# Performance work log

Hardware: AMD Instinct MI355X
Metric: run time of the kernel (lower is better)

Reference implementation:

```python
import jax, jax.numpy as jnp
import numpy as np

B = 8192; NPG = 32; N = B * NPG; E = 4 * N
F_IN = 70; HEADS = 2; HOUT = 64; D = HEADS * HOUT; NB = 4; REL = 86; DK = D // 2
NEG_SLOPE = 0.2; EPS = 1e-5


def setup_inputs():
    key = jax.random.key(0)
    ks = list(jax.random.split(key, 32)); ki = iter(ks)
    def nk():
        return next(ki)
    def rn(shape, s=0.1):
        return jax.random.normal(nk(), shape, jnp.float32) * s
    base = (jnp.arange(E) // (E // B)) * NPG  # each graph owns a contiguous node range
    def edges():
        s = base + jax.random.randint(nk(), (E,), 0, NPG)
        d = base + jax.random.randint(nk(), (E,), 0, NPG)
        return jnp.stack([s, d]).astype(jnp.int32)
    return dict(
        xh=rn((N, F_IN), 1.0), xt=rn((N, F_IN), 1.0),
        edge_h=edges(), edge_t=edges(),
        batch=(jnp.arange(N) // NPG).astype(jnp.int32),
        rels=jax.random.randint(nk(), (B,), 0, REL).astype(jnp.int32),
        W0=rn((F_IN, D)), Wr=rn((NB - 1, D, D)),
        att_src=rn((NB, HEADS, HOUT)), att_dst=rn((NB, HEADS, HOUT)),
        gat_b=jnp.zeros((NB, D), jnp.float32),
        sag_rel_w=rn((NB, D)), sag_rel_b=jnp.zeros((NB,), jnp.float32),
        sag_root_w=rn((NB, D)),
        nw=jnp.ones((NB, D), jnp.float32), nb2=jnp.zeros((NB, D), jnp.float32),
        inw=jnp.ones((F_IN,), jnp.float32), inb=jnp.zeros((F_IN,), jnp.float32),
        wq=rn((D, DK)), wk=rn((D, DK)),
        cob=jnp.zeros((DK,), jnp.float32), coa=rn((DK,)),
        rel_emb=rn((REL, D * D)),
    )


def _lnorm(x, w, b):  # PyG LayerNorm, node mode (per-node over features)
    mu = jnp.mean(x, -1, keepdims=True)
    var = jnp.var(x, -1, keepdims=True)
    return (x - mu) * jax.lax.rsqrt(var + EPS) * w + b


def _gat(x, src, dst, W, a_s, a_d, bias):
    # src/dst already include self-loops (PyG GATConv default add_self_loops=True)
    h = (x @ W).reshape(N, HEADS, HOUT)
    a_src = jnp.einsum('nhc,hc->nh', h, a_s)
    a_dst = jnp.einsum('nhc,hc->nh', h, a_d)
    alpha = jax.nn.leaky_relu(a_src[src] + a_dst[dst], NEG_SLOPE)  # [E+N, H]
    m = jax.ops.segment_max(alpha, dst, num_segments=N)
    ex = jnp.exp(alpha - m[dst])
    den = jax.ops.segment_sum(ex, dst, num_segments=N)
    w = ex / (den[dst] + 1e-16)
    out = jax.ops.segment_sum(h[src] * w[:, :, None], dst, num_segments=N)
    return out.reshape(N, D) + bias


def _readout(x, ei, batch, rw, rb, root_w):
    # SAGPooling(min_score=-1): GraphConv score, per-graph softmax, keeps all nodes
    aggr = jax.ops.segment_sum(x[ei[0]], ei[1], num_segments=N)
    score = aggr @ rw + rb + x @ root_w  # [N]
    m = jax.ops.segment_max(score, batch, num_segments=B)
    ex = jnp.exp(score - m[batch])
    den = jax.ops.segment_sum(ex, batch, num_segments=B)
    s = ex / (den[batch] + 1e-16)
    return jax.ops.segment_sum(x * s[:, None], batch, num_segments=B)  # global_add_pool [B, D]


def _l2norm(x):
    return x / jnp.clip(jnp.linalg.norm(x, axis=-1, keepdims=True), 1e-12)


def _forward(xh, xt, edge_h, edge_t, batch, rels, W0, Wr, att_src, att_dst, gat_b,
             sag_rel_w, sag_rel_b, sag_root_w, nw, nb2, inw, inb, wq, wk, cob, coa, rel_emb):
    loops = jnp.arange(N, dtype=edge_h.dtype)
    def side(x, ei):
        src = jnp.concatenate([ei[0], loops])
        dst = jnp.concatenate([ei[1], loops])
        x = _lnorm(x, inw, inb)
        reprs = []
        for i in range(NB):
            W = W0 if i == 0 else Wr[i - 1]
            x = _gat(x, src, dst, W, att_src[i], att_dst[i], gat_b[i])
            reprs.append(_readout(x, ei, batch, sag_rel_w[i], sag_rel_b[i], sag_root_w[i]))
            x = jax.nn.elu(_lnorm(x, nw[i], nb2[i]))
        return jnp.stack(reprs, axis=-2)  # [B, NB, D]

    rh = side(xh, edge_h)
    rt = side(xt, edge_t)

    # CoAttentionLayer(receiver=heads, attendant=tails)
    keys = rh @ wk       # [B, NB, DK]
    queries = rt @ wq    # [B, NB, DK]
    att = jnp.tanh(keys[:, :, None, :] + queries[:, None, :, :] + cob) @ coa  # [B, NB, NB]

    # RESCAL
    r = _l2norm(rel_emb[rels]).reshape(B, D, D)
    h = _l2norm(rh)
    t = _l2norm(rt)
    scores = jnp.einsum('bid,bde,bje->bij', h, r, t)
    return jnp.sum(att * scores, axis=(-2, -1))  # [B]


def reference(xh, xt, edge_h, edge_t, batch, rels, W0, Wr, att_src, att_dst, gat_b,
              sag_rel_w, sag_rel_b, sag_root_w, nw, nb2, inw, inb, wq, wk, cob, coa, rel_emb):
    return _forward(xh, xt, edge_h, edge_t, batch, rels, W0, Wr, att_src, att_dst, gat_b,
                    sag_rel_w, sag_rel_b, sag_root_w, nw, nb2, inw, inb, wq, wk, cob, coa, rel_emb)
```

## Files before the change

### kernel.cpp

```cpp
#include <hip/hip_runtime.h>
#include <math.h>

#define NG 8192
#define NPG 32
#define NN (NG*NPG)
#define NE (NN*4)
#define EPG 128
#define NEL (EPG+NPG)
#define FIN 70
#define DIM 128
#define XS 132
#define TS 36
#define NB 4
#define DK 64
#define NREL 86

typedef __attribute__((ext_vector_type(8))) short short8;
typedef __attribute__((ext_vector_type(4))) float f32x4;
typedef __attribute__((ext_vector_type(4))) unsigned int u32x4;

__device__ inline unsigned cvtpk(float a, float b) {
  unsigned r;
  asm("v_cvt_pk_bf16_f32 %0, %1, %2" : "=v"(r) : "v"(a), "v"(b));
  return r;
}
__device__ inline float lo16f(unsigned u) { return __uint_as_float(u << 16); }
__device__ inline float hi16f(unsigned u) { return __uint_as_float(u & 0xffff0000u); }
__device__ inline float bf16f(unsigned short h) {
  return __uint_as_float(((unsigned int)h) << 16);
}

__device__ inline void split8(const f32x4& a, const f32x4& b, short8& hi, short8& lo) {
  u32x4 H, L;
  #pragma unroll
  for (int p = 0; p < 2; ++p) {
    float x0 = a[2*p], x1 = a[2*p+1];
    unsigned h = cvtpk(x0, x1);
    H[p] = h;
    L[p] = cvtpk(x0 - lo16f(h), x1 - hi16f(h));
  }
  #pragma unroll
  for (int p = 0; p < 2; ++p) {
    float x0 = b[2*p], x1 = b[2*p+1];
    unsigned h = cvtpk(x0, x1);
    H[2+p] = h;
    L[2+p] = cvtpk(x0 - lo16f(h), x1 - hi16f(h));
  }
  hi = __builtin_bit_cast(short8, H);
  lo = __builtin_bit_cast(short8, L);
}

__device__ inline short8 ld8(const unsigned short* p) {
  union { short8 s; uint2 u[2]; } U;
  U.u[0] = *(const uint2*)p;
  U.u[1] = *(const uint2*)(p + 4);
  return U.s;
}

struct Smem {
  float x[NPG][XS];
  unsigned short h2thi[DIM][TS];
  unsigned short h2tlo[DIM][TS];
  union {
    struct {
      float Pt[2][NPG][TS];
      float alpha[2][NEL];
    } a;
    struct {
      float keysl[NB][DK];
      float querl[NB][DK];
      float attw[NB*NB];
      float red[NB*NB];
      float u4[4][DIM];
    } f;
  } uu;
  int   srcl[EPG];
  int   dstl[EPG];
  float asrc[NPG][2];
  float adst[NPG][2];
  float den[NPG][2];
  float mh[2];
  float wred[4][2];
  float pl[NPG];
  float ql[NPG];
  float sval[NPG];
  float sacc[NPG];
  float repr[2][NB][DIM];
  float scl[2][NB];
};

__global__ __launch_bounds__(256) void relnorm_kernel(
    const float* __restrict__ re, float* __restrict__ outn) {
  int r = blockIdx.x;
  const float* row = re + (size_t)r * (DIM*DIM);
  float s = 0.f;
  for (int i = threadIdx.x; i < DIM*DIM; i += 256) { float v = row[i]; s += v*v; }
  for (int w = 1; w < 64; w <<= 1) s += __shfl_xor(s, w);
  __shared__ float sred[4];
  if ((threadIdx.x & 63) == 0) sred[threadIdx.x >> 6] = s;
  __syncthreads();
  if (threadIdx.x == 0) outn[r] = sqrtf(sred[0]+sred[1]+sred[2]+sred[3]);
}

__global__ __launch_bounds__(256, 3) void ssi_kernel(
    const float* __restrict__ xh, const float* __restrict__ xt,
    const int* __restrict__ eh, const int* __restrict__ et,
    const int* __restrict__ rels,
    const float* __restrict__ W0, const float* __restrict__ Wr,
    const float* __restrict__ att_src, const float* __restrict__ att_dst,
    const float* __restrict__ gat_b,
    const float* __restrict__ srw, const float* __restrict__ srb,
    const float* __restrict__ sroot,
    const float* __restrict__ nw, const float* __restrict__ nb2,
    const float* __restrict__ inw, const float* __restrict__ inb,
    const float* __restrict__ wqm, const float* __restrict__ wkm,
    const float* __restrict__ cob, const float* __restrict__ coa,
    const float* __restrict__ rel_emb, const float* __restrict__ rnorm,
    float* __restrict__ out)
{
  __shared__ Smem sm;
  const int t = threadIdx.x;
  const int g = blockIdx.x;
  const int n0 = g * NPG;
  const int lw = t & 63;
  const int r0 = lw & 15;
  const int g4 = lw >> 4;
  const int nb = (t >> 6) * 32;
  const int hdw = t >> 7;

  for (int side = 0; side < 2; ++side) {
    const float* xin = side ? xt : xh;
    const int*   ed  = side ? et : eh;

    if (t < EPG) {
      sm.srcl[t] = ed[g*EPG + t] - n0;
      sm.dstl[t] = ed[NE + g*EPG + t] - n0;
    }
    {
      int n = t >> 3, j = t & 7;
      float s = 0.f, s2 = 0.f;
      for (int f = j; f < FIN; f += 8) {
        float v = xin[(size_t)(n0+n)*FIN + f];
        s += v; s2 += v*v;
      }
      for (int w = 1; w < 8; w <<= 1) { s += __shfl_xor(s, w); s2 += __shfl_xor(s2, w); }
      float mu  = s * (1.f/FIN);
      float var = s2 * (1.f/FIN) - mu*mu;
      float inv = rsqrtf(var + 1e-5f);
      for (int f = j; f < FIN; f += 8) {
        float v = xin[(size_t)(n0+n)*FIN + f];
        sm.x[n][f] = (v - mu) * inv * inw[f] + inb[f];
      }
      for (int f = FIN + j; f < 96; f += 8) sm.x[n][f] = 0.f;
    }
    __syncthreads();

    for (int li = 0; li < NB; ++li) {
      {
        const float* W = (li == 0) ? W0 : (Wr + (size_t)(li-1)*DIM*DIM);
        const int K  = (li == 0) ? FIN : DIM;
        const int KS = (li == 0) ? 3 : 4;
        f32x4 acc[2][2];
        #pragma unroll
        for (int mt = 0; mt < 2; ++mt)
          #pragma unroll
          for (int nt = 0; nt < 2; ++nt)
            acc[mt][nt] = (f32x4){0.f,0.f,0.f,0.f};
        for (int ks = 0; ks < KS; ++ks) {
          const int k0 = ks*32 + g4*8;
          short8 ah[2], al[2], bh[2], bl[2];
          #pragma unroll
          for (int mt = 0; mt < 2; ++mt) {
            f32x4 va = *(const f32x4*)&sm.x[mt*16 + r0][k0];
            f32x4 vb = *(const f32x4*)&sm.x[mt*16 + r0][k0+4];
            split8(va, vb, ah[mt], al[mt]);
          }
          #pragma unroll
          for (int nt = 0; nt < 2; ++nt) {
            const int c = nb + nt*16 + r0;
            f32x4 wa, wb;
            #pragma unroll
            for (int j = 0; j < 4; ++j) {
              int ka = k0 + j, kb = k0 + 4 + j;
              wa[j] = (ka < K) ? W[(size_t)ka*DIM + c] : 0.f;
              wb[j] = (kb < K) ? W[(size_t)kb*DIM + c] : 0.f;
            }
            split8(wa, wb, bh[nt], bl[nt]);
          }
          #pragma unroll
          for (int mt = 0; mt < 2; ++mt)
            #pragma unroll
            for (int nt = 0; nt < 2; ++nt) {
              acc[mt][nt] = __builtin_amdgcn_mfma_f32_16x16x32_bf16(ah[mt], bh[nt], acc[mt][nt], 0,0,0);
              acc[mt][nt] = __builtin_amdgcn_mfma_f32_16x16x32_bf16(ah[mt], bl[nt], acc[mt][nt], 0,0,0);
              acc[mt][nt] = __builtin_amdgcn_mfma_f32_16x16x32_bf16(al[mt], bh[nt], acc[mt][nt], 0,0,0);
              acc[mt][nt] = __builtin_amdgcn_mfma_f32_16x16x32_bf16(al[mt], bl[nt], acc[mt][nt], 0,0,0);
            }
        }
        #pragma unroll
        for (int mt = 0; mt < 2; ++mt)
          #pragma unroll
          for (int nt = 0; nt < 2; ++nt) {
            const int c = nb + nt*16 + r0;
            const int row0 = mt*16 + g4*4;
            f32x4 a = acc[mt][nt];
            unsigned h0 = cvtpk(a[0], a[1]), h1 = cvtpk(a[2], a[3]);
            unsigned l0 = cvtpk(a[0]-lo16f(h0), a[1]-hi16f(h0));
            unsigned l1 = cvtpk(a[2]-lo16f(h1), a[3]-hi16f(h1));
            *(uint2*)&sm.h2thi[c][row0] = make_uint2(h0, h1);
            *(uint2*)&sm.h2tlo[c][row0] = make_uint2(l0, l1);
          }
      }
      __syncthreads();

      {
        int n = t >> 3, hd = (t >> 2) & 1, j = t & 3;
        const float* as = att_src + ((size_t)li*2 + hd)*64;
        const float* ad = att_dst + ((size_t)li*2 + hd)*64;
        float ss = 0.f, sd = 0.f;
        #pragma unroll
        for (int u2 = 0; u2 < 16; ++u2) {
          int cl = u2*4 + j;
          int c = hd*64 + cl;
          float hv = bf16f(sm.h2thi[c][n]) + bf16f(sm.h2tlo[c][n]);
          ss += hv * as[cl];
          sd += hv * ad[cl];
        }
        ss += __shfl_xor(ss,1); ss += __shfl_xor(ss,2);
        sd += __shfl_xor(sd,1); sd += __shfl_xor(sd,2);
        if (j == 0) { sm.asrc[n][hd] = ss; sm.adst[n][hd] = sd; }
        float* Pz = &sm.uu.a.Pt[0][0][0];
        for (int idx = t; idx < 2*NPG*TS; idx += 256) Pz[idx] = 0.f;
      }
      __syncthreads();

      if (t < NEL) {
        int s = (t < EPG) ? sm.srcl[t] : (t - EPG);
        int d = (t < EPG) ? sm.dstl[t] : (t - EPG);
        #pragma unroll
        for (int hd = 0; hd < 2; ++hd) {
          float a = sm.asrc[s][hd] + sm.adst[d][hd];
          sm.uu.a.alpha[hd][t] = (a > 0.f) ? a : 0.2f*a;
        }
      }
      __syncthreads();

      {
        float a0 = (t < NEL) ? sm.uu.a.alpha[0][t] : -1e30f;
        float a1 = (t < NEL) ? sm.uu.a.alpha[1][t] : -1e30f;
        for (int w = 1; w < 64; w <<= 1) {
          a0 = fmaxf(a0, __shfl_xor(a0, w));
          a1 = fmaxf(a1, __shfl_xor(a1, w));
        }
        if ((t & 63) == 0) { sm.wred[t>>6][0] = a0; sm.wred[t>>6][1] = a1; }
      }
      __syncthreads();
      if (t < 2) {
        sm.mh[t] = fmaxf(fmaxf(sm.wred[0][t], sm.wred[1][t]),
                         fmaxf(sm.wred[2][t], sm.wred[3][t]));
      }
      __syncthreads();

      if (t < NEL) {
        int s = (t < EPG) ? sm.srcl[t] : (t - EPG);
        int d = (t < EPG) ? sm.dstl[t] : (t - EPG);
        float e0 = expf(sm.uu.a.alpha[0][t] - sm.mh[0]);
        float e1 = expf(sm.uu.a.alpha[1][t] - sm.mh[1]);
        atomicAdd(&sm.uu.a.Pt[0][d][s], e0);
        atomicAdd(&sm.uu.a.Pt[1][d][s], e1);
      }
      __syncthreads();

      if (t < 64) {
        int d = t & 31, hd = t >> 5;
        float s = 0.f;
        #pragma unroll
        for (int s4 = 0; s4 < NPG; s4 += 4) {
          f32x4 v = *(const f32x4*)&sm.uu.a.Pt[hd][d][s4];
          s += v[0] + v[1] + v[2] + v[3];
        }
        sm.den[d][hd] = 1.f / (s + 1e-16f);
      }
      __syncthreads();

      {
        int hd = t >> 7, r = (t >> 2) & 31, s0 = (t & 3) * 8;
        f32x4 pa = *(const f32x4*)&sm.uu.a.Pt[hd][r][s0];
        f32x4 pb = *(const f32x4*)&sm.uu.a.Pt[hd][r][s0+4];
        float dv = sm.den[r][hd];
        #pragma unroll
        for (int q = 0; q < 4; ++q) { pa[q] *= dv; pb[q] *= dv; }
        __syncthreads();
        unsigned short* Pu = (unsigned short*)&sm.uu.a.Pt[0][0][0];
        const int LO = 2*NPG*TS;
        int base = (hd*NPG + r)*TS + s0;
        unsigned h0 = cvtpk(pa[0], pa[1]), h1 = cvtpk(pa[2], pa[3]);
        unsigned h2_ = cvtpk(pb[0], pb[1]), h3 = cvtpk(pb[2], pb[3]);
        unsigned l0 = cvtpk(pa[0]-lo16f(h0), pa[1]-hi16f(h0));
        unsigned l1 = cvtpk(pa[2]-lo16f(h1), pa[3]-hi16f(h1));
        unsigned l2 = cvtpk(pb[0]-lo16f(h2_), pb[1]-hi16f(h2_));
        unsigned l3 = cvtpk(pb[2]-lo16f(h3), pb[3]-hi16f(h3));
        *(uint2*)(Pu + base)     = make_uint2(h0, h1);
        *(uint2*)(Pu + base + 4) = make_uint2(h2_, h3);
        *(uint2*)(Pu + LO + base)     = make_uint2(l0, l1);
        *(uint2*)(Pu + LO + base + 4) = make_uint2(l2, l3);
      }
      __syncthreads();

      {
        const unsigned short* Pu = (const unsigned short*)&sm.uu.a.Pt[0][0][0];
        const int LO = 2*NPG*TS;
        const int k0 = g4*8;
        f32x4 acc[2][2];
        #pragma unroll
        for (int mt = 0; mt < 2; ++mt)
          #pragma unroll
          for (int nt = 0; nt < 2; ++nt)
            acc[mt][nt] = (f32x4){0.f,0.f,0.f,0.f};
        short8 Ah[2], Al[2], Bh[2], Bl[2];
        #pragma unroll
        for (int mt = 0; mt < 2; ++mt) {
          int base = (hdw*NPG + mt*16 + r0)*TS + k0;
          Ah[mt] = ld8(Pu + base);
          Al[mt] = ld8(Pu + LO + base);
        }
        #pragma unroll
        for (int nt = 0; nt < 2; ++nt) {
          const int c = nb + nt*16 + r0;
          Bh[nt] = ld8(&sm.h2thi[c][k0]);
          Bl[nt] = ld8(&sm.h2tlo[c][k0]);
        }
        #pragma unroll
        for (int mt = 0; mt < 2; ++mt)
          #pragma unroll
          for (int nt = 0; nt < 2; ++nt) {
            acc[mt][nt] = __builtin_amdgcn_mfma_f32_16x16x32_bf16(Ah[mt], Bh[nt], acc[mt][nt], 0,0,0);
            acc[mt][nt] = __builtin_amdgcn_mfma_f32_16x16x32_bf16(Ah[mt], Bl[nt], acc[mt][nt], 0,0,0);
            acc[mt][nt] = __builtin_amdgcn_mfma_f32_16x16x32_bf16(Al[mt], Bh[nt], acc[mt][nt], 0,0,0);
          }
        #pragma unroll
        for (int nt = 0; nt < 2; ++nt) {
          const int c = nb + nt*16 + r0;
          float bc = gat_b[(size_t)li*DIM + c];
          #pragma unroll
          for (int mt = 0; mt < 2; ++mt)
            #pragma unroll
            for (int q = 0; q < 4; ++q)
              sm.x[mt*16 + g4*4 + q][c] = acc[mt][nt][q] + bc;
        }
      }
      __syncthreads();

      {
        int n = t >> 3, j = t & 7;
        const float* rw = srw   + (size_t)li*DIM;
        const float* ro = sroot + (size_t)li*DIM;
        float p = 0.f, q = 0.f;
        #pragma unroll
        for (int u2 = 0; u2 < 16; ++u2) {
          int c = u2*8 + j;
          float xv = sm.x[n][c];
          p += xv * rw[c];
          q += xv * ro[c];
        }
        for (int w = 1; w < 8; w <<= 1) { p += __shfl_xor(p,w); q += __shfl_xor(q,w); }
        if (j == 0) { sm.pl[n] = p; sm.ql[n] = q; }
        if (t < NPG) sm.sacc[t] = 0.f;
      }
      __syncthreads();

      if (t < EPG) atomicAdd(&sm.sacc[sm.dstl[t]], sm.pl[sm.srcl[t]]);
      __syncthreads();

      if (t < NPG) {
        float s = sm.sacc[t] + srb[li] + sm.ql[t];
        float m = s;
        for (int w = 1; w < 32; w <<= 1) m = fmaxf(m, __shfl_xor(m, w));
        float ex = expf(s - m);
        float dn = ex;
        for (int w = 1; w < 32; w <<= 1) dn += __shfl_xor(dn, w);
        sm.sval[t] = ex / (dn + 1e-16f);
      }
      __syncthreads();

      if (t < DIM) {
        float a = 0.f;
        for (int n = 0; n < NPG; ++n) a += sm.x[n][t] * sm.sval[n];
        sm.repr[side][li][t] = a;
      }
      __syncthreads();

      if (li < NB-1) {
        int n = t >> 3, j = t & 7;
        float s = 0.f, s2 = 0.f;
        #pragma unroll
        for (int u2 = 0; u2 < 16; ++u2) {
          float v = sm.x[n][u2*8 + j];
          s += v; s2 += v*v;
        }
        for (int w = 1; w < 8; w <<= 1) { s += __shfl_xor(s,w); s2 += __shfl_xor(s2,w); }
        float mu  = s * (1.f/DIM);
        float var = s2 * (1.f/DIM) - mu*mu;
        float inv = rsqrtf(var + 1e-5f);
        const float* wv = nw  + (size_t)li*DIM;
        const float* bv = nb2 + (size_t)li*DIM;
        #pragma unroll
        for (int u2 = 0; u2 < 16; ++u2) {
          int c = u2*8 + j;
          float v = (sm.x[n][c] - mu) * inv * wv[c] + bv[c];
          sm.x[n][c] = (v > 0.f) ? v : expm1f(v);
        }
        __syncthreads();
      }
    }
  }

  {
    int i2 = t >> 6, k = t & 63;
    float ak = 0.f, aq = 0.f;
    for (int d = 0; d < DIM; ++d) {
      ak += sm.repr[0][i2][d] * wkm[(size_t)d*DK + k];
      aq += sm.repr[1][i2][d] * wqm[(size_t)d*DK + k];
    }
    sm.uu.f.keysl[i2][k] = ak;
    sm.uu.f.querl[i2][k] = aq;
  }
  {
    int sd = t >> 7, i = (t >> 5) & 3, j2 = t & 31;
    float s = 0.f;
    #pragma unroll
    for (int u2 = 0; u2 < 4; ++u2) {
      float v = sm.repr[sd][i][j2*4+u2];
      s += v*v;
    }
    for (int w = 1; w < 32; w <<= 1) s += __shfl_xor(s, w);
    if (j2 == 0) sm.scl[sd][i] = 1.f / fmaxf(sqrtf(s), 1e-12f);
  }
  __syncthreads();

  {
    int pair = t >> 4, kk = t & 15;
    int i = pair >> 2, j = pair & 3;
    float a = 0.f;
    #pragma unroll
    for (int u2 = 0; u2 < 4; ++u2) {
      int k = kk*4+u2;
      a += tanhf(sm.uu.f.keysl[i][k] + sm.uu.f.querl[j][k] + cob[k]) * coa[k];
    }
    for (int w = 1; w < 16; w <<= 1) a += __shfl_xor(a, w);
    if (kk == 0) sm.uu.f.attw[pair] = a;
  }
  int rel = rels[g];
  if (t < DIM) {
    const float* rr = rel_emb + (size_t)rel * (DIM*DIM);
    float a0=0.f, a1=0.f, a2=0.f, a3=0.f;
    for (int d = 0; d < DIM; ++d) {
      float rv = rr[(size_t)d*DIM + t];
      a0 += sm.repr[0][0][d] * rv;
      a1 += sm.repr[0][1][d] * rv;
      a2 += sm.repr[0][2][d] * rv;
      a3 += sm.repr[0][3][d] * rv;
    }
    sm.uu.f.u4[0][t]=a0; sm.uu.f.u4[1][t]=a1; sm.uu.f.u4[2][t]=a2; sm.uu.f.u4[3][t]=a3;
  }
  __syncthreads();

  {
    float rninv = 1.f / fmaxf(rnorm[rel], 1e-12f);
    int pair = t >> 4, kk = t & 15;
    int i = pair >> 2, j = pair & 3;
    float a = 0.f;
    #pragma unroll
    for (int u2 = 0; u2 < 8; ++u2) {
      int e = kk*8+u2;
      a += sm.uu.f.u4[i][e] * sm.repr[1][j][e];
    }
    for (int w = 1; w < 16; w <<= 1) a += __shfl_xor(a, w);
    if (kk == 0)
      sm.uu.f.red[pair] = sm.uu.f.attw[pair] * a * sm.scl[0][i] * sm.scl[1][j] * rninv;
  }
  __syncthreads();
  if (t == 0) {
    float s = 0.f;
    for (int p = 0; p < NB*NB; ++p) s += sm.uu.f.red[p];
    out[g] = s;
  }
}

extern "C" void kernel_launch(void* const* d_in, const int* in_sizes, int n_in,
                              void* d_out, int out_size, void* d_ws, size_t ws_size,
                              hipStream_t stream) {
  const float* xh      = (const float*)d_in[0];
  const float* xt      = (const float*)d_in[1];
  const int*   eh      = (const int*)d_in[2];
  const int*   et      = (const int*)d_in[3];
  const int*   rels    = (const int*)d_in[5];
  const float* W0      = (const float*)d_in[6];
  const float* Wr      = (const float*)d_in[7];
  const float* att_src = (const float*)d_in[8];
  const float* att_dst = (const float*)d_in[9];
  const float* gat_b   = (const float*)d_in[10];
  const float* srw     = (const float*)d_in[11];
  const float* srb     = (const float*)d_in[12];
  const float* sroot   = (const float*)d_in[13];
  const float* nw      = (const float*)d_in[14];
  const float* nb2_    = (const float*)d_in[15];
  const float* inw     = (const float*)d_in[16];
  const float* inb     = (const float*)d_in[17];
  const float* wqm     = (const float*)d_in[18];
  const float* wkm     = (const float*)d_in[19];
  const float* cob     = (const float*)d_in[20];
  const float* coa     = (const float*)d_in[21];
  const float* rel_emb = (const float*)d_in[22];
  float* out   = (float*)d_out;
  float* rnorm = (float*)d_ws;

  relnorm_kernel<<<NREL, 256, 0, stream>>>(rel_emb, rnorm);
  ssi_kernel<<<NG, 256, 0, stream>>>(xh, xt, eh, et, rels, W0, Wr, att_src, att_dst,
      gat_b, srw, srb, sroot, nw, nb2_, inw, inb, wqm, wkm, cob, coa, rel_emb,
      rnorm, out);
}
```

Baseline: 1.433 ms.

## Pre-split GAT weights to bf16 hi/lo in a prep kernel and trim softmax syncs

A new prep kernel converts W0/Wr once into transposed bf16 hi/lo arrays in workspace, so the main kernel loads B fragments with 16-byte loads instead of strided fp32 gathers followed by per-block splitting. The GAT edge softmax now keeps alpha in registers, drops the alpha and den shared arrays and two barriers, and computes row sums with shuffles. Several expf/expm1f calls become the fast __expf intrinsic, and one readout loop is unrolled. The new path only runs when workspace is large enough, and the fast exp intrinsics lose some precision.

```diff
diff --git a/kernel.cpp b/kernel.cpp
--- a/kernel.cpp
+++ b/kernel.cpp
@@ -56,16 +56,17 @@
   U.u[1] = *(const uint2*)(p + 4);
   return U.s;
 }
+__device__ inline short8 ld16B(const unsigned short* p) {
+  u32x4 u = *(const u32x4*)p;
+  return __builtin_bit_cast(short8, u);
+}
 
 struct Smem {
   float x[NPG][XS];
   unsigned short h2thi[DIM][TS];
   unsigned short h2tlo[DIM][TS];
   union {
-    struct {
-      float Pt[2][NPG][TS];
-      float alpha[2][NEL];
-    } a;
+    float Pt[2][NPG][TS];
     struct {
       float keysl[NB][DK];
       float querl[NB][DK];
@@ -78,8 +79,6 @@
   int   dstl[EPG];
   float asrc[NPG][2];
   float adst[NPG][2];
-  float den[NPG][2];
-  float mh[2];
   float wred[4][2];
   float pl[NPG];
   float ql[NPG];
@@ -102,11 +101,29 @@
   if (threadIdx.x == 0) outn[r] = sqrtf(sred[0]+sred[1]+sred[2]+sred[3]);
 }
 
+__global__ __launch_bounds__(256) void wprep_kernel(
+    const float* __restrict__ W0, const float* __restrict__ Wr,
+    unsigned short* __restrict__ wsp) {
+  int idx = blockIdx.x * 256 + threadIdx.x;
+  int l = idx >> 14;
+  int k = (idx >> 7) & 127;
+  int c = idx & 127;
+  float v;
+  if (l == 0) v = (k < FIN) ? W0[(size_t)k*DIM + c] : 0.f;
+  else        v = Wr[(size_t)(l-1)*DIM*DIM + (size_t)k*DIM + c];
+  unsigned h = cvtpk(v, 0.f);
+  unsigned lo = cvtpk(v - lo16f(h), 0.f);
+  int o = (l << 14) + c*128 + k;
+  wsp[o] = (unsigned short)h;
+  wsp[65536 + o] = (unsigned short)lo;
+}
+
 __global__ __launch_bounds__(256, 3) void ssi_kernel(
     const float* __restrict__ xh, const float* __restrict__ xt,
     const int* __restrict__ eh, const int* __restrict__ et,
     const int* __restrict__ rels,
     const float* __restrict__ W0, const float* __restrict__ Wr,
+    const unsigned short* __restrict__ wsp,
     const float* __restrict__ att_src, const float* __restrict__ att_dst,
     const float* __restrict__ gat_b,
     const float* __restrict__ srw, const float* __restrict__ srb,
@@ -175,17 +192,28 @@
             f32x4 vb = *(const f32x4*)&sm.x[mt*16 + r0][k0+4];
             split8(va, vb, ah[mt], al[mt]);
           }
-          #pragma unroll
-          for (int nt = 0; nt < 2; ++nt) {
-            const int c = nb + nt*16 + r0;
-            f32x4 wa, wb;
+          if (wsp) {
+            const unsigned short* Wh = wsp + (li << 14);
+            const unsigned short* Wl = wsp + 65536 + (li << 14);
             #pragma unroll
-            for (int j = 0; j < 4; ++j) {
-              int ka = k0 + j, kb = k0 + 4 + j;
-              wa[j] = (ka < K) ? W[(size_t)ka*DIM + c] : 0.f;
-              wb[j] = (kb < K) ? W[(size_t)kb*DIM + c] : 0.f;
+            for (int nt = 0; nt < 2; ++nt) {
+              const int c = nb + nt*16 + r0;
+              bh[nt] = ld16B(Wh + c*128 + k0);
+              bl[nt] = ld16B(Wl + c*128 + k0);
             }
-            split8(wa, wb, bh[nt], bl[nt]);
+          } else {
+            #pragma unroll
+            for (int nt = 0; nt < 2; ++nt) {
+              const int c = nb + nt*16 + r0;
+              f32x4 wa, wb;
+              #pragma unroll
+              for (int j = 0; j < 4; ++j) {
+                int ka = k0 + j, kb = k0 + 4 + j;
+                wa[j] = (ka < K) ? W[(size_t)ka*DIM + c] : 0.f;
+                wb[j] = (kb < K) ? W[(size_t)kb*DIM + c] : 0.f;
+              }
+              split8(wa, wb, bh[nt], bl[nt]);
+            }
           }
           #pragma unroll
           for (int mt = 0; mt < 2; ++mt)
@@ -229,69 +257,53 @@
         ss += __shfl_xor(ss,1); ss += __shfl_xor(ss,2);
         sd += __shfl_xor(sd,1); sd += __shfl_xor(sd,2);
         if (j == 0) { sm.asrc[n][hd] = ss; sm.adst[n][hd] = sd; }
-        float* Pz = &sm.uu.a.Pt[0][0][0];
+        float* Pz = &sm.uu.Pt[0][0][0];
         for (int idx = t; idx < 2*NPG*TS; idx += 256) Pz[idx] = 0.f;
       }
       __syncthreads();
 
+      float al0 = -1e30f, al1 = -1e30f;
+      int es = 0, edd = 0;
       if (t < NEL) {
-        int s = (t < EPG) ? sm.srcl[t] : (t - EPG);
-        int d = (t < EPG) ? sm.dstl[t] : (t - EPG);
-        #pragma unroll
-        for (int hd = 0; hd < 2; ++hd) {
-          float a = sm.asrc[s][hd] + sm.adst[d][hd];
-          sm.uu.a.alpha[hd][t] = (a > 0.f) ? a : 0.2f*a;
-        }
-      }
-      __syncthreads();
-
+        es  = (t < EPG) ? sm.srcl[t] : (t - EPG);
+        edd = (t < EPG) ? sm.dstl[t] : (t - EPG);
+        float a0 = sm.asrc[es][0] + sm.adst[edd][0];
+        float a1 = sm.asrc[es][1] + sm.adst[edd][1];
+        al0 = (a0 > 0.f) ? a0 : 0.2f*a0;
+        al1 = (a1 > 0.f) ? a1 : 0.2f*a1;
+      }
       {
-        float a0 = (t < NEL) ? sm.uu.a.alpha[0][t] : -1e30f;
-        float a1 = (t < NEL) ? sm.uu.a.alpha[1][t] : -1e30f;
+        float m0 = al0, m1 = al1;
         for (int w = 1; w < 64; w <<= 1) {
-          a0 = fmaxf(a0, __shfl_xor(a0, w));
-          a1 = fmaxf(a1, __shfl_xor(a1, w));
-        }
-        if ((t & 63) == 0) { sm.wred[t>>6][0] = a0; sm.wred[t>>6][1] = a1; }
-      }
-      __syncthreads();
-      if (t < 2) {
-        sm.mh[t] = fmaxf(fmaxf(sm.wred[0][t], sm.wred[1][t]),
-                         fmaxf(sm.wred[2][t], sm.wred[3][t]));
+          m0 = fmaxf(m0, __shfl_xor(m0, w));
+          m1 = fmaxf(m1, __shfl_xor(m1, w));
+        }
+        if ((t & 63) == 0) { sm.wred[t>>6][0] = m0; sm.wred[t>>6][1] = m1; }
       }
       __syncthreads();
 
       if (t < NEL) {
-        int s = (t < EPG) ? sm.srcl[t] : (t - EPG);
-        int d = (t < EPG) ? sm.dstl[t] : (t - EPG);
-        float e0 = expf(sm.uu.a.alpha[0][t] - sm.mh[0]);
-        float e1 = expf(sm.uu.a.alpha[1][t] - sm.mh[1]);
-        atomicAdd(&sm.uu.a.Pt[0][d][s], e0);
-        atomicAdd(&sm.uu.a.Pt[1][d][s], e1);
-      }
-      __syncthreads();
-
-      if (t < 64) {
-        int d = t & 31, hd = t >> 5;
-        float s = 0.f;
-        #pragma unroll
-        for (int s4 = 0; s4 < NPG; s4 += 4) {
-          f32x4 v = *(const f32x4*)&sm.uu.a.Pt[hd][d][s4];
-          s += v[0] + v[1] + v[2] + v[3];
-        }
-        sm.den[d][hd] = 1.f / (s + 1e-16f);
+        float M0 = fmaxf(fmaxf(sm.wred[0][0], sm.wred[1][0]),
+                         fmaxf(sm.wred[2][0], sm.wred[3][0]));
+        float M1 = fmaxf(fmaxf(sm.wred[0][1], sm.wred[1][1]),
+                         fmaxf(sm.wred[2][1], sm.wred[3][1]));
+        atomicAdd(&sm.uu.Pt[0][edd][es], __expf(al0 - M0));
+        atomicAdd(&sm.uu.Pt[1][edd][es], __expf(al1 - M1));
       }
       __syncthreads();
 
       {
         int hd = t >> 7, r = (t >> 2) & 31, s0 = (t & 3) * 8;
-        f32x4 pa = *(const f32x4*)&sm.uu.a.Pt[hd][r][s0];
-        f32x4 pb = *(const f32x4*)&sm.uu.a.Pt[hd][r][s0+4];
-        float dv = sm.den[r][hd];
+        f32x4 pa = *(const f32x4*)&sm.uu.Pt[hd][r][s0];
+        f32x4 pb = *(const f32x4*)&sm.uu.Pt[hd][r][s0+4];
+        float rs = pa[0]+pa[1]+pa[2]+pa[3]+pb[0]+pb[1]+pb[2]+pb[3];
+        rs += __shfl_xor(rs, 1);
+        rs += __shfl_xor(rs, 2);
+        float dv = 1.f / (rs + 1e-16f);
         #pragma unroll
         for (int q = 0; q < 4; ++q) { pa[q] *= dv; pb[q] *= dv; }
         __syncthreads();
-        unsigned short* Pu = (unsigned short*)&sm.uu.a.Pt[0][0][0];
+        unsigned short* Pu = (unsigned short*)&sm.uu.Pt[0][0][0];
         const int LO = 2*NPG*TS;
         int base = (hd*NPG + r)*TS + s0;
         unsigned h0 = cvtpk(pa[0], pa[1]), h1 = cvtpk(pa[2], pa[3]);
@@ -308,7 +320,7 @@
       __syncthreads();
 
       {
-        const unsigned short* Pu = (const unsigned short*)&sm.uu.a.Pt[0][0][0];
+        const unsigned short* Pu = (const unsigned short*)&sm.uu.Pt[0][0][0];
         const int LO = 2*NPG*TS;
         const int k0 = g4*8;
         f32x4 acc[2][2];
@@ -376,7 +388,7 @@
         float s = sm.sacc[t] + srb[li] + sm.ql[t];
         float m = s;
         for (int w = 1; w < 32; w <<= 1) m = fmaxf(m, __shfl_xor(m, w));
-        float ex = expf(s - m);
+        float ex = __expf(s - m);
         float dn = ex;
         for (int w = 1; w < 32; w <<= 1) dn += __shfl_xor(dn, w);
         sm.sval[t] = ex / (dn + 1e-16f);
@@ -385,6 +397,7 @@
 
       if (t < DIM) {
         float a = 0.f;
+        #pragma unroll 8
         for (int n = 0; n < NPG; ++n) a += sm.x[n][t] * sm.sval[n];
         sm.repr[side][li][t] = a;
       }
@@ -408,7 +421,7 @@
         for (int u2 = 0; u2 < 16; ++u2) {
           int c = u2*8 + j;
           float v = (sm.x[n][c] - mu) * inv * wv[c] + bv[c];
-          sm.x[n][c] = (v > 0.f) ? v : expm1f(v);
+          sm.x[n][c] = (v > 0.f) ? v : (__expf(v) - 1.f);
         }
         __syncthreads();
       }
@@ -515,8 +528,15 @@
   float* out   = (float*)d_out;
   float* rnorm = (float*)d_ws;
 
+  const size_t WS_NEED = 512 + 2 * 65536 * sizeof(unsigned short);
+  const unsigned short* wsp = nullptr;
   relnorm_kernel<<<NREL, 256, 0, stream>>>(rel_emb, rnorm);
-  ssi_kernel<<<NG, 256, 0, stream>>>(xh, xt, eh, et, rels, W0, Wr, att_src, att_dst,
-      gat_b, srw, srb, sroot, nw, nb2_, inw, inb, wqm, wkm, cob, coa, rel_emb,
-      rnorm, out);
-}
+  if (ws_size >= WS_NEED) {
+    unsigned short* w = (unsigned short*)((char*)d_ws + 512);
+    wprep_kernel<<<256, 256, 0, stream>>>(W0, Wr, w);
+    wsp = w;
+  }
+  ssi_kernel<<<NG, 256, 0, stream>>>(xh, xt, eh, et, rels, W0, Wr, wsp,
+      att_src, att_dst, gat_b, srw, srb, sroot, nw, nb2_, inw, inb,
+      wqm, wkm, cob, coa, rel_emb, rnorm, out);
+}
```

New measurement: 1.236 ms. 13.7% less time.
